# Kernel tuning notes

Hardware: AMD Instinct MI355X
Metric: run time of the kernel (lower is better)

The kernel has to match this reference:

```python
import jax, jax.numpy as jnp
import numpy as np

N, E, C5, C6, H = 50000, 100000, 8000, 12000, 128
RE, R5, R6 = 2 * E, 5 * C5, 6 * C6
BN_EPS = 1e-5


def _bn_relu(x, g, b):
    # BatchNorm1d (training-mode batch stats, biased var) + ReLU
    m = x.mean(0)
    xc = x - m
    v = (xc * xc).mean(0)
    return jax.nn.relu(xc * jax.lax.rsqrt(v + BN_EPS) * g + b)


def _mlp2(x, w1, g1, b1, w2, g2, b2):
    h = _bn_relu(x @ w1, g1, b1)
    return _bn_relu(h @ w2, g2, b2)


def _gather11(x, src_nodes, src_inst, n_inst, tgt_nodes):
    # ptens 1b->1b gather (channel multiplier 2):
    #  part A: identity map on shared atoms, summed over overlapping sources
    #  part B: broadcast of source-instance sum to shared atoms
    pa = jax.ops.segment_sum(x, src_nodes, num_segments=N)[tgt_nodes]
    s = jax.ops.segment_sum(x, src_inst, num_segments=n_inst)
    pb = jax.ops.segment_sum(s[src_inst], src_nodes, num_segments=N)[tgt_nodes]
    return jnp.concatenate([pa, pb], -1)


def _forward(node_rep, edge_rep, cycle_rep, edge_nodes, c5_nodes, c6_nodes, P):
    (nm_w1, nm_g1, nm_b1, nm_w2, nm_g2, nm_b2,
     em_w1, em_g1, em_b1, em_w2, em_g2, em_b2,
     ce_w1, ce_g1, ce_b1, ce_w2, ce_g2, ce_b2,
     cm_w1, cm_g1, cm_b1, cm_w2, cm_g2, cm_b2,
     fm_w, fm_g, fm_b) = P
    edge_inst = jnp.arange(RE, dtype=jnp.int32) // 2
    c5_inst = jnp.arange(R5, dtype=jnp.int32) // 5
    c6_inst = jnp.arange(R6, dtype=jnp.int32) // 6
    cyc_nodes = jnp.concatenate([c5_nodes, c6_nodes])
    cyc_inst = jnp.concatenate([c5_inst, c6_inst + C5])

    # ---- Edge_node ----
    n2e = node_rep[edge_nodes]                                        # 0b->1b(edge), h
    n2e = _gather11(n2e, edge_nodes, edge_inst, E, edge_nodes)        # 2h
    e2e = _gather11(edge_rep, edge_nodes, edge_inst, E, edge_nodes)   # 2h
    e2e = _gather11(e2e, edge_nodes, edge_inst, E, edge_nodes)        # 4h
    e2n = jax.ops.segment_sum(jnp.concatenate([e2e, n2e], -1), edge_nodes, num_segments=N)  # 1b->0b, 6h
    edge_out1 = _mlp2(jnp.concatenate([edge_rep, e2e, n2e], -1),
                      em_w1, em_g1, em_b1, em_w2, em_g2, em_b2)       # [RE, h]
    node_out = _mlp2(jnp.concatenate([node_rep, e2n], -1),
                     nm_w1, nm_g1, nm_b1, nm_w2, nm_g2, nm_b2)        # [N, h]

    # ---- Edge_Cycle ----
    e2c5 = _gather11(edge_rep, edge_nodes, edge_inst, E, c5_nodes)    # 2h
    e2c5 = _gather11(e2c5, c5_nodes, c5_inst, C5, c5_nodes)           # 4h
    e2c6 = _gather11(edge_rep, edge_nodes, edge_inst, E, c6_nodes)    # 2h
    e2c6 = _gather11(e2c6, c6_nodes, c6_inst, C6, c6_nodes)           # 4h
    cycle_in = jnp.concatenate([e2c5, e2c6], 0)                       # row-cat: [R5+R6, 4h]
    cycle_new = jnp.concatenate([cycle_in, cycle_rep], -1)            # 5h
    c2e = _gather11(cycle_new, cyc_nodes, cyc_inst, C5 + C6, edge_nodes)  # 10h
    edge_out2 = _mlp2(jnp.concatenate([edge_rep, c2e], -1),
                      ce_w1, ce_g1, ce_b1, ce_w2, ce_g2, ce_b2)       # [RE, h]
    cycle_out = _mlp2(cycle_new, cm_w1, cm_g1, cm_b1, cm_w2, cm_g2, cm_b2)  # [R5+R6, h]

    edge_out = _bn_relu(jnp.concatenate([edge_out1, edge_out2], -1) @ fm_w, fm_g, fm_b)
    return node_out, edge_out, cycle_out


def setup_inputs() -> dict:
    key = jax.random.key(0)
    ks = jax.random.split(key, 16)
    d = {}
    d["node_rep"] = jax.random.normal(ks[0], (N, H), jnp.float32)
    d["edge_rep"] = jax.random.normal(ks[1], (RE, H), jnp.float32)
    d["cycle_rep"] = jax.random.normal(ks[2], (R5 + R6, H), jnp.float32)
    d["edge_nodes"] = jax.random.randint(ks[3], (RE,), 0, N, jnp.int32)
    d["c5_nodes"] = jax.random.randint(ks[4], (R5,), 0, N, jnp.int32)
    d["c6_nodes"] = jax.random.randint(ks[5], (R6,), 0, N, jnp.int32)
    i = [6]
    def w(shape):
        out = jax.random.normal(ks[i[0]], shape, jnp.float32) / np.float32(np.sqrt(shape[0]))
        i[0] += 1
        return out
    for p, fin in (("nm", 7 * H), ("em", 7 * H), ("ce", 11 * H), ("cm", 5 * H)):
        d[p + "_w1"] = w((fin, 2 * H)); d[p + "_g1"] = jnp.ones((2 * H,), jnp.float32); d[p + "_b1"] = jnp.zeros((2 * H,), jnp.float32)
        d[p + "_w2"] = w((2 * H, H)); d[p + "_g2"] = jnp.ones((H,), jnp.float32); d[p + "_b2"] = jnp.zeros((H,), jnp.float32)
    d["fm_w"] = w((2 * H, H)); d["fm_g"] = jnp.ones((H,), jnp.float32); d["fm_b"] = jnp.zeros((H,), jnp.float32)
    return d


def reference(node_rep, edge_rep, cycle_rep, edge_nodes, c5_nodes, c6_nodes,
              nm_w1, nm_g1, nm_b1, nm_w2, nm_g2, nm_b2,
              em_w1, em_g1, em_b1, em_w2, em_g2, em_b2,
              ce_w1, ce_g1, ce_b1, ce_w2, ce_g2, ce_b2,
              cm_w1, cm_g1, cm_b1, cm_w2, cm_g2, cm_b2,
              fm_w, fm_g, fm_b):
    P = (nm_w1, nm_g1, nm_b1, nm_w2, nm_g2, nm_b2,
         em_w1, em_g1, em_b1, em_w2, em_g2, em_b2,
         ce_w1, ce_g1, ce_b1, ce_w2, ce_g2, ce_b2,
         cm_w1, cm_g1, cm_b1, cm_w2, cm_g2, cm_b2,
         fm_w, fm_g, fm_b)
    return _forward(node_rep, edge_rep, cycle_rep, edge_nodes, c5_nodes, c6_nodes, P)
```

## Files before the change

kernel.cpp:

```cpp
#include <hip/hip_runtime.h>
#include <cstdint>
#include <cstddef>
#include <initializer_list>

typedef short bf16x8 __attribute__((ext_vector_type(8)));
typedef float f32x4 __attribute__((ext_vector_type(4)));

__device__ inline float bf2f(unsigned short h) { return __uint_as_float(((unsigned)h) << 16); }
__device__ inline unsigned short f2bf(float f) {
  unsigned u = __float_as_uint(f);
  u += 0x7fff + ((u >> 16) & 1);
  return (unsigned short)(u >> 16);
}

struct Seg { const void* base; const int* idx; const float* scale; int ld; int wk; int bf16;
             const float* bnsc; const float* bnsh; };
struct GemmArgs { Seg segs[7]; const float* addB; const int* addIdx; float* stats; };

__global__ void k_count(float* dst, const int* __restrict__ idx, int R) {
  int r = blockIdx.x * 256 + threadIdx.x;
  if (r < R) atomicAdd(&dst[idx[r]], 1.0f);
}

__global__ void k_scales(const float* __restrict__ deg, const float* __restrict__ d5,
                         const float* __restrict__ d6, float* deg2, float* dd, int n) {
  int i = blockIdx.x * 256 + threadIdx.x;
  if (i < n) {
    float d = deg[i]; deg2[i] = d * d;
    float a = d5[i], b = d6[i]; dd[i] = a * a + b * b;
  }
}

__global__ void k_wtrans(const float* __restrict__ W, unsigned short* __restrict__ Wt,
                         int K, int CN) {
  int t = blockIdx.x * 256 + threadIdx.x;
  if (t >= K * CN) return;
  int k = t / CN, n = t - k * CN;
  Wt[(size_t)n * K + k] = f2bf(W[t]);
}

__global__ void k_gsum(float* __restrict__ out, int outLd,
                       const float* __restrict__ T, int tLd,
                       const float* __restrict__ scale, const int* __restrict__ idx,
                       int k, int nInst) {
  int t = blockIdx.x * 256 + threadIdx.x;
  int c = t >> 7, ch = t & 127;
  if (c >= nInst) return;
  float acc = 0.f;
  int b0 = c * k;
  for (int j = 0; j < k; ++j) {
    int rid = idx ? idx[b0 + j] : b0 + j;
    float v = T[(size_t)rid * tLd + ch];
    if (scale) v *= scale[rid];
    acc += v;
  }
  out[(size_t)c * outLd + ch] = acc;
}

__global__ void k_scatter(float* __restrict__ dst, const float* __restrict__ src,
                          const int* __restrict__ idx, int R, int C, int div) {
  int r = blockIdx.x;
  if (r >= R) return;
  int n = idx[r];
  const float* s = src + (size_t)(r / div) * C;
  float* d = dst + (size_t)n * C;
  for (int c = threadIdx.x; c < C; c += blockDim.x)
    atomicAdd(&d[c], s[c]);
}

__global__ void k_bnfin(float* __restrict__ coef, const float* __restrict__ stats,
                        const float* __restrict__ g, const float* __restrict__ b,
                        int M, int C) {
  int c = threadIdx.x;
  if (c >= C) return;
  float inv = 1.f / (float)M;
  float m = stats[c] * inv;
  float v = stats[C + c] * inv - m * m;
  float s = g[c] * rsqrtf(v + 1e-5f);
  coef[c] = s;
  coef[C + c] = b[c] - m * s;
}

template <int OUT_BF16>
__launch_bounds__(256)
__global__ void k_gemm(GemmArgs ga, const unsigned short* __restrict__ Wt, int Ktot,
                       int K, int CN, void* __restrict__ Cp, int M) {
  __shared__ char AsB[2 * 128 * 64];
  __shared__ char BsB[2 * 128 * 64];
  int tid = threadIdx.x;
  int row0 = blockIdx.x * 128, col0 = blockIdx.y * 128;
  int l = tid & 63, w = tid >> 6;
  int wm = w >> 1, wn = w & 1;
  int lr = l & 15, g = l >> 4;
  int chunkOff = (g ^ ((lr >> 1) & 3)) << 4;
  int sm = tid >> 2;
  int sc4 = tid & 3;
  f32x4 acc[4][4] = {};

  uint4 pa0[2], pa1[2], pb[2];
  float psc[2];
  float4 c0, c1, c2, c3;

  auto issue = [&](int k0n) {
    Seg sg = ga.segs[k0n >> 7];
    int kin = k0n & 127;
#pragma unroll
    for (int h = 0; h < 2; ++h) {
      int m = sm + 64 * h;
      int grow = row0 + m;
      uint4 z4 = make_uint4(0, 0, 0, 0);
      pa0[h] = z4; pa1[h] = z4; psc[h] = 1.f;
      if (grow < M) {
        int rid = sg.idx ? sg.idx[grow] : grow;
        if (sg.bf16) {
          pa0[h] = *(const uint4*)((const unsigned short*)sg.base + (size_t)rid * sg.ld + kin + sc4 * 8);
        } else {
          const float* fp = (const float*)sg.base + (size_t)rid * sg.ld + kin + sc4 * 8;
          pa0[h] = *(const uint4*)fp;
          pa1[h] = *(const uint4*)(fp + 4);
          if (sg.scale) psc[h] = sg.scale[rid];
        }
      }
      pb[h] = *(const uint4*)(Wt + (size_t)(col0 + m) * Ktot + sg.wk + kin + sc4 * 8);
    }
    if (sg.bnsc) {
      const float* sp = sg.bnsc + kin + sc4 * 8;
      const float* hp = sg.bnsh + kin + sc4 * 8;
      c0 = *(const float4*)sp; c1 = *(const float4*)(sp + 4);
      c2 = *(const float4*)hp; c3 = *(const float4*)(hp + 4);
    }
  };

  issue(0);
  int buf = 0;
  for (int k0 = 0; k0 < K; k0 += 32) {
    {
      Seg sg = ga.segs[k0 >> 7];
      char* sA = AsB + buf * 8192;
      char* sB = BsB + buf * 8192;
#pragma unroll
      for (int h = 0; h < 2; ++h) {
        int m = sm + 64 * h;
        uint4 pk;
        if (sg.bf16) {
          pk = pa0[h];
          if (sg.bnsc) {
            unsigned short* u = (unsigned short*)&pk;
            float cs0[8] = {c0.x, c0.y, c0.z, c0.w, c1.x, c1.y, c1.z, c1.w};
            float sh0[8] = {c2.x, c2.y, c2.z, c2.w, c3.x, c3.y, c3.z, c3.w};
#pragma unroll
            for (int e = 0; e < 8; ++e) {
              float f = fmaxf(0.f, bf2f(u[e]) * cs0[e] + sh0[e]);
              u[e] = f2bf(f);
            }
          }
        } else {
          float4 v0 = *(const float4*)&pa0[h];
          float4 v1 = *(const float4*)&pa1[h];
          float s = psc[h];
          v0.x *= s; v0.y *= s; v0.z *= s; v0.w *= s;
          v1.x *= s; v1.y *= s; v1.z *= s; v1.w *= s;
          if (sg.bnsc) {
            v0.x = fmaxf(0.f, v0.x * c0.x + c2.x);
            v0.y = fmaxf(0.f, v0.y * c0.y + c2.y);
            v0.z = fmaxf(0.f, v0.z * c0.z + c2.z);
            v0.w = fmaxf(0.f, v0.w * c0.w + c2.w);
            v1.x = fmaxf(0.f, v1.x * c1.x + c3.x);
            v1.y = fmaxf(0.f, v1.y * c1.y + c3.y);
            v1.z = fmaxf(0.f, v1.z * c1.z + c3.z);
            v1.w = fmaxf(0.f, v1.w * c1.w + c3.w);
          }
          pk.x = f2bf(v0.x) | ((unsigned)f2bf(v0.y) << 16);
          pk.y = f2bf(v0.z) | ((unsigned)f2bf(v0.w) << 16);
          pk.z = f2bf(v1.x) | ((unsigned)f2bf(v1.y) << 16);
          pk.w = f2bf(v1.z) | ((unsigned)f2bf(v1.w) << 16);
        }
        *(uint4*)(sA + m * 64 + ((sc4 ^ ((m >> 1) & 3)) << 4)) = pk;
        *(uint4*)(sB + m * 64 + ((sc4 ^ ((m >> 1) & 3)) << 4)) = pb[h];
      }
    }
    __syncthreads();
    if (k0 + 32 < K) issue(k0 + 32);
    const char* lA = AsB + buf * 8192;
    const char* lB = BsB + buf * 8192;
    bf16x8 a[4], b4[4];
#pragma unroll
    for (int i = 0; i < 4; ++i) {
      int m = wm * 64 + i * 16 + lr;
      a[i] = *(const bf16x8*)(lA + m * 64 + chunkOff);
    }
#pragma unroll
    for (int j = 0; j < 4; ++j) {
      int n = wn * 64 + j * 16 + lr;
      b4[j] = *(const bf16x8*)(lB + n * 64 + chunkOff);
    }
#pragma unroll
    for (int i = 0; i < 4; ++i)
#pragma unroll
      for (int j = 0; j < 4; ++j)
        acc[i][j] = __builtin_amdgcn_mfma_f32_16x16x32_bf16(a[i], b4[j], acc[i][j], 0, 0, 0);
    buf ^= 1;
  }

  float csum[4] = {0.f, 0.f, 0.f, 0.f}, cqum[4] = {0.f, 0.f, 0.f, 0.f};
#pragma unroll
  for (int i = 0; i < 4; ++i) {
#pragma unroll
    for (int r = 0; r < 4; ++r) {
      int grow = row0 + wm * 64 + i * 16 + g * 4 + r;
      if (grow >= M) continue;
      const float* zr = nullptr;
      if (ga.addB) {
        int rid = ga.addIdx ? ga.addIdx[grow] : grow;
        zr = ga.addB + (size_t)rid * 256;
      }
#pragma unroll
      for (int j = 0; j < 4; ++j) {
        int col = col0 + wn * 64 + j * 16 + lr;
        float o = acc[i][j][r];
        if (zr) o += zr[col];
        csum[j] += o; cqum[j] += o * o;
        if (OUT_BF16) ((unsigned short*)Cp)[(size_t)grow * CN + col] = f2bf(o);
        else          ((float*)Cp)[(size_t)grow * CN + col] = o;
      }
    }
  }
  if (ga.stats) {
#pragma unroll
    for (int j = 0; j < 4; ++j) {
      float s = csum[j], q = cqum[j];
      s += __shfl_xor(s, 16); q += __shfl_xor(q, 16);
      s += __shfl_xor(s, 32); q += __shfl_xor(q, 32);
      if (g == 0) {
        int col = col0 + wn * 64 + j * 16 + lr;
        atomicAdd(&ga.stats[col], s);
        atomicAdd(&ga.stats[CN + col], q);
      }
    }
  }
}

template <int SB, int DB>
__global__ void k_bnapply(void* __restrict__ dst, const void* __restrict__ yv,
                          const float* __restrict__ g, const float* __restrict__ b,
                          const float* __restrict__ stats, int M, int C) {
  int t = blockIdx.x * 256 + threadIdx.x;
  if (t >= M * C) return;
  int c = t & (C - 1);
  float inv = 1.0f / (float)M;
  float m = stats[c] * inv;
  float v = stats[C + c] * inv - m * m;
  float sc = g[c] * rsqrtf(v + 1e-5f);
  float sh = b[c] - m * sc;
  float x = SB ? bf2f(((const unsigned short*)yv)[t]) : ((const float*)yv)[t];
  x = x * sc + sh;
  x = x > 0.f ? x : 0.f;
  if (DB) ((unsigned short*)dst)[t] = f2bf(x);
  else    ((float*)dst)[t] = x;
}

extern "C" void kernel_launch(void* const* d_in, const int* in_sizes, int n_in,
                              void* d_out, int out_size, void* d_ws, size_t ws_size,
                              hipStream_t stream) {
  constexpr int N = 50000, E = 100000, C5 = 8000, C6 = 12000;
  constexpr int RE = 2 * E, R5 = 5 * C5, R6 = 6 * C6, NC = R5 + R6, CC = C5 + C6;

  const float* node_rep  = (const float*)d_in[0];
  const float* edge_rep  = (const float*)d_in[1];
  const float* cycle_rep = (const float*)d_in[2];
  const int* en  = (const int*)d_in[3];
  const int* cn5 = (const int*)d_in[4];
  const int* cn6 = (const int*)d_in[5];
  const float* nm_w1 = (const float*)d_in[6],  *nm_g1 = (const float*)d_in[7],  *nm_b1 = (const float*)d_in[8];
  const float* nm_w2 = (const float*)d_in[9],  *nm_g2 = (const float*)d_in[10], *nm_b2 = (const float*)d_in[11];
  const float* em_w1 = (const float*)d_in[12], *em_g1 = (const float*)d_in[13], *em_b1 = (const float*)d_in[14];
  const float* em_w2 = (const float*)d_in[15], *em_g2 = (const float*)d_in[16], *em_b2 = (const float*)d_in[17];
  const float* ce_w1 = (const float*)d_in[18], *ce_g1 = (const float*)d_in[19], *ce_b1 = (const float*)d_in[20];
  const float* ce_w2 = (const float*)d_in[21], *ce_g2 = (const float*)d_in[22], *ce_b2 = (const float*)d_in[23];
  const float* cm_w1 = (const float*)d_in[24], *cm_g1 = (const float*)d_in[25], *cm_b1 = (const float*)d_in[26];
  const float* cm_w2 = (const float*)d_in[27], *cm_g2 = (const float*)d_in[28], *cm_b2 = (const float*)d_in[29];
  const float* fm_w  = (const float*)d_in[30], *fm_g  = (const float*)d_in[31], *fm_b  = (const float*)d_in[32];
  float* outD = (float*)d_out;
  float* outN = outD;
  float* outE = outD + (size_t)N * 128;
  float* outC = outD + (size_t)(N + RE) * 128;

  char* wsb = (char*)d_ws;
  size_t off = 0;
  auto A = [&](size_t bytes) { void* p = wsb + off; off += (bytes + 255) & ~(size_t)255; return p; };
  float* deg = (float*)A(N * 4);
  float* d5  = (float*)A(N * 4);
  float* d6  = (float*)A(N * 4);
  float* Ae  = (float*)A((size_t)N * 128 * 4);
  float* Be  = (float*)A((size_t)N * 128 * 4);
  float* Bn  = (float*)A((size_t)N * 128 * 4);
  float* pb2 = (float*)A((size_t)N * 256 * 4);
  float* pb5 = (float*)A((size_t)N * 256 * 4);
  float* pb6 = (float*)A((size_t)N * 256 * 4);
  float* Ac  = (float*)A((size_t)N * 128 * 4);
  size_t zeroBytes = off;
  float* deg2 = (float*)A(N * 4);
  float* dd   = (float*)A(N * 4);
  float* Z    = (float*)A((size_t)N * 256 * 4);
  float* stats = (float*)A(512 * 4);
  float* coefCe1 = (float*)A(512 * 4);
  float* coefCe2 = (float*)A(512 * 4);
  float* coefEm1 = (float*)A(512 * 4);
  float* coefEm2 = (float*)A(512 * 4);
  float* coefNm1 = (float*)A(512 * 4);
  float* coefCm1 = (float*)A(512 * 4);
  unsigned short* WtNm1 = (unsigned short*)A((size_t)896 * 256 * 2);
  unsigned short* WtEm1 = (unsigned short*)A((size_t)896 * 256 * 2);
  unsigned short* WtCe1 = (unsigned short*)A((size_t)1408 * 256 * 2);
  unsigned short* WtCm1 = (unsigned short*)A((size_t)640 * 256 * 2);
  unsigned short* WtNm2 = (unsigned short*)A((size_t)256 * 128 * 2);
  unsigned short* WtEm2 = (unsigned short*)A((size_t)256 * 128 * 2);
  unsigned short* WtCe2 = (unsigned short*)A((size_t)256 * 128 * 2);
  unsigned short* WtCm2 = (unsigned short*)A((size_t)256 * 128 * 2);
  unsigned short* WtFm  = (unsigned short*)A((size_t)256 * 128 * 2);
  char*  Yb   = (char*)A((size_t)RE * 256 * 2);
  unsigned short* O2 = (unsigned short*)A((size_t)RE * 128 * 2);
  if (off > ws_size) return;

  float* s2 = (float*)Yb;
  float* sN = s2 + (size_t)E * 128;
  float* s3 = (float*)Yb;
  float* s5 = (float*)Yb;
  float* s6 = s5 + (size_t)C5 * 256;
  float* scb = (float*)Yb;
  float* Ysc = scb + (size_t)CC * 640;

  auto gsum = [&](float* o, int oLd, const float* T, int tLd,
                  const float* scl, const int* idx, int k, int nInst) {
    int tot = nInst * 128;
    k_gsum<<<(tot + 255) / 256, 256, 0, stream>>>(o, oLd, T, tLd, scl, idx, k, nInst);
  };
  auto scat = [&](float* dst, const float* src, const int* idx, int R, int C, int dv) {
    k_scatter<<<R, 128, 0, stream>>>(dst, src, idx, R, C, dv);
  };
  auto wtr = [&](const float* W, unsigned short* Wt, int K, int CN) {
    k_wtrans<<<(K * CN + 255) / 256, 256, 0, stream>>>(W, Wt, K, CN);
  };
  auto gemm = [&](std::initializer_list<Seg> segs, const unsigned short* Wt, int Ktot,
                  int CN, void* Co, int M, bool outBf, const float* addB, const int* addIdx,
                  float* st) {
    GemmArgs ga{}; int i = 0;
    for (const Seg& s : segs) ga.segs[i++] = s;
    ga.addB = addB; ga.addIdx = addIdx; ga.stats = st;
    int K = i * 128;
    dim3 g((M + 127) / 128, CN / 128);
    if (outBf) k_gemm<1><<<g, 256, 0, stream>>>(ga, Wt, Ktot, K, CN, Co, M);
    else       k_gemm<0><<<g, 256, 0, stream>>>(ga, Wt, Ktot, K, CN, Co, M);
  };
  auto zstat = [&](int C) { hipMemsetAsync(stats, 0, 2 * C * sizeof(float), stream); };
  auto fin = [&](float* coef, const float* g, const float* b, int M, int C) {
    k_bnfin<<<1, 256, 0, stream>>>(coef, stats, g, b, M, C);
  };
  auto apply = [&](void* dst, const void* y, const float* g, const float* b,
                   int M, int C, int sb, int db) {
    int tot = M * C, gb = (tot + 255) / 256;
    if (sb && db)       k_bnapply<1, 1><<<gb, 256, 0, stream>>>(dst, y, g, b, stats, M, C);
    else if (sb && !db) k_bnapply<1, 0><<<gb, 256, 0, stream>>>(dst, y, g, b, stats, M, C);
    else if (!sb && db) k_bnapply<0, 1><<<gb, 256, 0, stream>>>(dst, y, g, b, stats, M, C);
    else                k_bnapply<0, 0><<<gb, 256, 0, stream>>>(dst, y, g, b, stats, M, C);
  };

  hipMemsetAsync(d_ws, 0, zeroBytes, stream);
  k_count<<<(RE + 255) / 256, 256, 0, stream>>>(deg, en, RE);
  k_count<<<(R5 + 255) / 256, 256, 0, stream>>>(d5, cn5, R5);
  k_count<<<(R6 + 255) / 256, 256, 0, stream>>>(d6, cn6, R6);
  k_scales<<<(N + 255) / 256, 256, 0, stream>>>(deg, d5, d6, deg2, dd, N);
  wtr(nm_w1, WtNm1, 896, 256);  wtr(em_w1, WtEm1, 896, 256);
  wtr(ce_w1, WtCe1, 1408, 256); wtr(cm_w1, WtCm1, 640, 256);
  wtr(nm_w2, WtNm2, 256, 128);  wtr(em_w2, WtEm2, 256, 128);
  wtr(ce_w2, WtCe2, 256, 128);  wtr(cm_w2, WtCm2, 256, 128);
  wtr(fm_w,  WtFm,  256, 128);

  gsum(s2, 128, edge_rep, 128, nullptr, nullptr, 2, E);
  gsum(sN, 128, node_rep, 128, nullptr, en, 2, E);
  scat(Ae, edge_rep, en, RE, 128, 1);
  scat(Be, s2, en, RE, 128, 2);
  scat(Bn, sN, en, RE, 128, 2);
  gsum(s3, 256, Ae, 128, nullptr, en, 2, E);
  gsum(s3 + 128, 256, Be, 128, nullptr, en, 2, E);
  scat(pb2, s3, en, RE, 256, 2);

  gsum(s5, 256, Ae, 128, nullptr, cn5, 5, C5);
  gsum(s5 + 128, 256, Be, 128, nullptr, cn5, 5, C5);
  gsum(s6, 256, Ae, 128, nullptr, cn6, 6, C6);
  gsum(s6 + 128, 256, Be, 128, nullptr, cn6, 6, C6);
  scat(pb5, s5, cn5, R5, 256, 5);
  scat(pb6, s6, cn6, R6, 256, 6);
  scat(Ac, cycle_rep, cn5, R5, 128, 1);
  scat(Ac, cycle_rep + (size_t)R5 * 128, cn6, R6, 128, 1);

  gsum(scb + 0,   640, Ae, 128, d5, cn5, 5, C5);
  gsum(scb + 128, 640, Be, 128, d5, cn5, 5, C5);
  gsum(scb + 256, 640, pb5, 256, nullptr, cn5, 5, C5);
  gsum(scb + 384, 640, pb5 + 128, 256, nullptr, cn5, 5, C5);
  gsum(scb + 512, 640, cycle_rep, 128, nullptr, nullptr, 5, C5);
  float* sc6 = scb + (size_t)C5 * 640;
  gsum(sc6 + 0,   640, Ae, 128, d6, cn6, 6, C6);
  gsum(sc6 + 128, 640, Be, 128, d6, cn6, 6, C6);
  gsum(sc6 + 256, 640, pb6, 256, nullptr, cn6, 6, C6);
  gsum(sc6 + 384, 640, pb6 + 128, 256, nullptr, cn6, 6, C6);
  gsum(sc6 + 512, 640, cycle_rep + (size_t)R5 * 128, 128, nullptr, nullptr, 6, C6);
  gemm({{scb, nullptr, nullptr, 640, 768, 0}, {scb + 128, nullptr, nullptr, 640, 896, 0},
        {scb + 256, nullptr, nullptr, 640, 1024, 0}, {scb + 384, nullptr, nullptr, 640, 1152, 0},
        {scb + 512, nullptr, nullptr, 640, 1280, 0}},
       WtCe1, 1408, 256, Ysc, CC, false, nullptr, nullptr, nullptr);
  gemm({{Ae, nullptr, dd, 128, 128, 0}, {Be, nullptr, dd, 128, 256, 0},
        {pb5, nullptr, d5, 256, 384, 0}, {pb5 + 128, nullptr, d5, 256, 512, 0},
        {pb6, nullptr, d6, 256, 384, 0}, {pb6 + 128, nullptr, d6, 256, 512, 0},
        {Ac, nullptr, nullptr, 128, 640, 0}},
       WtCe1, 1408, 256, Z, N, false, nullptr, nullptr, nullptr);
  scat(Z, Ysc, cn5, R5, 256, 5);
  scat(Z, Ysc + (size_t)C5 * 256, cn6, R6, 256, 6);
  zstat(256);
  gemm({{edge_rep, nullptr, nullptr, 128, 0, 0}}, WtCe1, 1408, 256, Yb, RE, true, Z, en, stats);
  fin(coefCe1, ce_g1, ce_b1, RE, 256);
  zstat(128);
  gemm({{Yb, nullptr, nullptr, 256, 0, 1, coefCe1, coefCe1 + 256},
        {Yb + 256, nullptr, nullptr, 256, 128, 1, coefCe1 + 128, coefCe1 + 384}},
       WtCe2, 256, 128, O2, RE, true, nullptr, nullptr, stats);
  fin(coefCe2, ce_g2, ce_b2, RE, 128);

  gemm({{Ae, nullptr, deg, 128, 128, 0}, {Be, nullptr, deg, 128, 256, 0},
        {pb2, nullptr, nullptr, 256, 384, 0}, {pb2 + 128, nullptr, nullptr, 256, 512, 0},
        {node_rep, nullptr, deg, 128, 640, 0}, {Bn, nullptr, nullptr, 128, 768, 0}},
       WtEm1, 896, 256, Z, N, false, nullptr, nullptr, nullptr);
  zstat(256);
  gemm({{edge_rep, nullptr, nullptr, 128, 0, 0}}, WtEm1, 896, 256, Yb, RE, true, Z, en, stats);
  fin(coefEm1, em_g1, em_b1, RE, 256);
  zstat(128);
  gemm({{Yb, nullptr, nullptr, 256, 0, 1, coefEm1, coefEm1 + 256},
        {Yb + 256, nullptr, nullptr, 256, 128, 1, coefEm1 + 128, coefEm1 + 384}},
       WtEm2, 256, 128, outE, RE, false, nullptr, nullptr, stats);
  fin(coefEm2, em_g2, em_b2, RE, 128);

  zstat(256);
  gemm({{node_rep, nullptr, nullptr, 128, 0, 0}, {Ae, nullptr, deg2, 128, 128, 0},
        {Be, nullptr, deg2, 128, 256, 0}, {pb2, nullptr, deg, 256, 384, 0},
        {pb2 + 128, nullptr, deg, 256, 512, 0}, {node_rep, nullptr, deg2, 128, 640, 0},
        {Bn, nullptr, deg, 128, 768, 0}},
       WtNm1, 896, 256, Yb, N, true, nullptr, nullptr, stats);
  fin(coefNm1, nm_g1, nm_b1, N, 256);
  zstat(128);
  gemm({{Yb, nullptr, nullptr, 256, 0, 1, coefNm1, coefNm1 + 256},
        {Yb + 256, nullptr, nullptr, 256, 128, 1, coefNm1 + 128, coefNm1 + 384}},
       WtNm2, 256, 128, outN, N, false, nullptr, nullptr, stats);
  apply(outN, outN, nm_g2, nm_b2, N, 128, 0, 0);

  gemm({{Ae, nullptr, d5, 128, 0, 0}, {Be, nullptr, d5, 128, 128, 0},
        {pb5, nullptr, nullptr, 256, 256, 0}, {pb5 + 128, nullptr, nullptr, 256, 384, 0}},
       WtCm1, 640, 256, Z, N, false, nullptr, nullptr, nullptr);
  zstat(256);
  gemm({{cycle_rep, nullptr, nullptr, 128, 512, 0}}, WtCm1, 640, 256, Yb, R5, true, Z, cn5, stats);
  gemm({{Ae, nullptr, d6, 128, 0, 0}, {Be, nullptr, d6, 128, 128, 0},
        {pb6, nullptr, nullptr, 256, 256, 0}, {pb6 + 128, nullptr, nullptr, 256, 384, 0}},
       WtCm1, 640, 256, Z, N, false, nullptr, nullptr, nullptr);
  gemm({{cycle_rep + (size_t)R5 * 128, nullptr, nullptr, 128, 512, 0}}, WtCm1, 640, 256,
       Yb + (size_t)R5 * 256 * 2, R6, true, Z, cn6, stats);
  fin(coefCm1, cm_g1, cm_b1, NC, 256);
  zstat(128);
  gemm({{Yb, nullptr, nullptr, 256, 0, 1, coefCm1, coefCm1 + 256},
        {Yb + 256, nullptr, nullptr, 256, 128, 1, coefCm1 + 128, coefCm1 + 384}},
       WtCm2, 256, 128, outC, NC, false, nullptr, nullptr, stats);
  apply(outC, outC, cm_g2, cm_b2, NC, 128, 0, 0);

  zstat(128);
  gemm({{outE, nullptr, nullptr, 128, 0, 0, coefEm2, coefEm2 + 128},
        {O2, nullptr, nullptr, 128, 128, 1, coefCe2, coefCe2 + 128}},
       WtFm, 256, 128, Yb, RE, true, nullptr, nullptr, stats);
  apply(outE, Yb, fm_g, fm_b, RE, 128, 1, 0);
}
```

Measured before the change: 3.385 ms.

## Shard BN stat atomics, store gather tables in bf16, fuse gather-sum-scatter kernels

```diff
diff --git a/kernel.cpp b/kernel.cpp
--- a/kernel.cpp
+++ b/kernel.cpp
@@ -15,7 +15,7 @@
 
 struct Seg { const void* base; const int* idx; const float* scale; int ld; int wk; int bf16;
              const float* bnsc; const float* bnsh; };
-struct GemmArgs { Seg segs[7]; const float* addB; const int* addIdx; float* stats; };
+struct GemmArgs { Seg segs[7]; const float* addB; const int* addIdx; float* stats; int addBf16; };
 
 __global__ void k_count(float* dst, const int* __restrict__ idx, int R) {
   int r = blockIdx.x * 256 + threadIdx.x;
@@ -37,6 +37,17 @@
   if (t >= K * CN) return;
   int k = t / CN, n = t - k * CN;
   Wt[(size_t)n * K + k] = f2bf(W[t]);
+}
+
+__global__ void k_cvt(unsigned short* __restrict__ dst, const float* __restrict__ src, int n8) {
+  int i = blockIdx.x * 256 + threadIdx.x;
+  if (i >= n8) return;
+  const float4* s = (const float4*)(src + (size_t)i * 8);
+  float4 a = s[0], b = s[1];
+  union { unsigned short u[8]; uint4 v; } o;
+  o.u[0] = f2bf(a.x); o.u[1] = f2bf(a.y); o.u[2] = f2bf(a.z); o.u[3] = f2bf(a.w);
+  o.u[4] = f2bf(b.x); o.u[5] = f2bf(b.y); o.u[6] = f2bf(b.z); o.u[7] = f2bf(b.w);
+  *(uint4*)(dst + (size_t)i * 8) = o.v;
 }
 
 __global__ void k_gsum(float* __restrict__ out, int outLd,
@@ -57,6 +68,26 @@
   out[(size_t)c * outLd + ch] = acc;
 }
 
+__global__ void k_gsc(float* __restrict__ dst, const float* __restrict__ T1,
+                      const float* __restrict__ T2, const int* __restrict__ gidx,
+                      const int* __restrict__ sidx, int k, int nInst, int cshift) {
+  int t = blockIdx.x * 256 + threadIdx.x;
+  int c = t >> cshift;
+  int C = 1 << cshift;
+  int ch = t & (C - 1);
+  if (c >= nInst) return;
+  const float* T = (ch < 128) ? T1 : T2;
+  int ch7 = ch & 127;
+  float acc = 0.f;
+  int b0 = c * k;
+  for (int j = 0; j < k; ++j) {
+    int rid = gidx ? gidx[b0 + j] : b0 + j;
+    acc += T[(size_t)rid * 128 + ch7];
+  }
+  for (int j = 0; j < k; ++j)
+    atomicAdd(&dst[(size_t)sidx[b0 + j] * C + ch], acc);
+}
+
 __global__ void k_scatter(float* __restrict__ dst, const float* __restrict__ src,
                           const int* __restrict__ idx, int R, int C, int div) {
   int r = blockIdx.x;
@@ -73,12 +104,14 @@
                         int M, int C) {
   int c = threadIdx.x;
   if (c >= C) return;
+  float s = 0.f, q = 0.f;
+  for (int sh = 0; sh < 16; ++sh) { s += stats[sh * 512 + c]; q += stats[sh * 512 + 256 + c]; }
   float inv = 1.f / (float)M;
-  float m = stats[c] * inv;
-  float v = stats[C + c] * inv - m * m;
-  float s = g[c] * rsqrtf(v + 1e-5f);
-  coef[c] = s;
-  coef[C + c] = b[c] - m * s;
+  float m = s * inv;
+  float v = q * inv - m * m;
+  float sc = g[c] * rsqrtf(v + 1e-5f);
+  coef[c] = sc;
+  coef[C + c] = b[c] - m * sc;
 }
 
 template <int OUT_BF16>
@@ -209,16 +242,19 @@
     for (int r = 0; r < 4; ++r) {
       int grow = row0 + wm * 64 + i * 16 + g * 4 + r;
       if (grow >= M) continue;
-      const float* zr = nullptr;
+      const float* zrF = nullptr;
+      const unsigned short* zrH = nullptr;
       if (ga.addB) {
         int rid = ga.addIdx ? ga.addIdx[grow] : grow;
-        zr = ga.addB + (size_t)rid * 256;
+        if (ga.addBf16) zrH = (const unsigned short*)ga.addB + (size_t)rid * 256;
+        else            zrF = ga.addB + (size_t)rid * 256;
       }
 #pragma unroll
       for (int j = 0; j < 4; ++j) {
         int col = col0 + wn * 64 + j * 16 + lr;
         float o = acc[i][j][r];
-        if (zr) o += zr[col];
+        if (zrF) o += zrF[col];
+        if (zrH) o += bf2f(zrH[col]);
         csum[j] += o; cqum[j] += o * o;
         if (OUT_BF16) ((unsigned short*)Cp)[(size_t)grow * CN + col] = f2bf(o);
         else          ((float*)Cp)[(size_t)grow * CN + col] = o;
@@ -226,6 +262,7 @@
     }
   }
   if (ga.stats) {
+    int shard = (blockIdx.x & 15) * 512;
 #pragma unroll
     for (int j = 0; j < 4; ++j) {
       float s = csum[j], q = cqum[j];
@@ -233,8 +270,8 @@
       s += __shfl_xor(s, 32); q += __shfl_xor(q, 32);
       if (g == 0) {
         int col = col0 + wn * 64 + j * 16 + lr;
-        atomicAdd(&ga.stats[col], s);
-        atomicAdd(&ga.stats[CN + col], q);
+        atomicAdd(&ga.stats[shard + col], s);
+        atomicAdd(&ga.stats[shard + 256 + col], q);
       }
     }
   }
@@ -242,18 +279,12 @@
 
 template <int SB, int DB>
 __global__ void k_bnapply(void* __restrict__ dst, const void* __restrict__ yv,
-                          const float* __restrict__ g, const float* __restrict__ b,
-                          const float* __restrict__ stats, int M, int C) {
+                          const float* __restrict__ coef, int M, int C) {
   int t = blockIdx.x * 256 + threadIdx.x;
   if (t >= M * C) return;
   int c = t & (C - 1);
-  float inv = 1.0f / (float)M;
-  float m = stats[c] * inv;
-  float v = stats[C + c] * inv - m * m;
-  float sc = g[c] * rsqrtf(v + 1e-5f);
-  float sh = b[c] - m * sc;
   float x = SB ? bf2f(((const unsigned short*)yv)[t]) : ((const float*)yv)[t];
-  x = x * sc + sh;
+  x = x * coef[c] + coef[C + c];
   x = x > 0.f ? x : 0.f;
   if (DB) ((unsigned short*)dst)[t] = f2bf(x);
   else    ((float*)dst)[t] = x;
@@ -302,13 +333,16 @@
   float* deg2 = (float*)A(N * 4);
   float* dd   = (float*)A(N * 4);
   float* Z    = (float*)A((size_t)N * 256 * 4);
-  float* stats = (float*)A(512 * 4);
+  float* stats = (float*)A(16 * 512 * 4);
   float* coefCe1 = (float*)A(512 * 4);
   float* coefCe2 = (float*)A(512 * 4);
   float* coefEm1 = (float*)A(512 * 4);
   float* coefEm2 = (float*)A(512 * 4);
   float* coefNm1 = (float*)A(512 * 4);
+  float* coefNm2 = (float*)A(512 * 4);
   float* coefCm1 = (float*)A(512 * 4);
+  float* coefCm2 = (float*)A(512 * 4);
+  float* coefFm  = (float*)A(512 * 4);
   unsigned short* WtNm1 = (unsigned short*)A((size_t)896 * 256 * 2);
   unsigned short* WtEm1 = (unsigned short*)A((size_t)896 * 256 * 2);
   unsigned short* WtCe1 = (unsigned short*)A((size_t)1408 * 256 * 2);
@@ -322,11 +356,8 @@
   unsigned short* O2 = (unsigned short*)A((size_t)RE * 128 * 2);
   if (off > ws_size) return;
 
-  float* s2 = (float*)Yb;
-  float* sN = s2 + (size_t)E * 128;
-  float* s3 = (float*)Yb;
-  float* s5 = (float*)Yb;
-  float* s6 = s5 + (size_t)C5 * 256;
+  unsigned short* Zb = (unsigned short*)Ac;
+
   float* scb = (float*)Yb;
   float* Ysc = scb + (size_t)CC * 640;
 
@@ -335,6 +366,12 @@
     int tot = nInst * 128;
     k_gsum<<<(tot + 255) / 256, 256, 0, stream>>>(o, oLd, T, tLd, scl, idx, k, nInst);
   };
+  auto gsc = [&](float* dst, const float* T1, const float* T2, const int* gidx,
+                 const int* sidx, int k, int nInst) {
+    int cshift = T2 ? 8 : 7;
+    int tot = nInst << cshift;
+    k_gsc<<<(tot + 255) / 256, 256, 0, stream>>>(dst, T1, T2, gidx, sidx, k, nInst, cshift);
+  };
   auto scat = [&](float* dst, const float* src, const int* idx, int R, int C, int dv) {
     k_scatter<<<R, 128, 0, stream>>>(dst, src, idx, R, C, dv);
   };
@@ -343,26 +380,25 @@
   };
   auto gemm = [&](std::initializer_list<Seg> segs, const unsigned short* Wt, int Ktot,
                   int CN, void* Co, int M, bool outBf, const float* addB, const int* addIdx,
-                  float* st) {
+                  int addBf, float* st) {
     GemmArgs ga{}; int i = 0;
     for (const Seg& s : segs) ga.segs[i++] = s;
-    ga.addB = addB; ga.addIdx = addIdx; ga.stats = st;
+    ga.addB = addB; ga.addIdx = addIdx; ga.stats = st; ga.addBf16 = addBf;
     int K = i * 128;
     dim3 g((M + 127) / 128, CN / 128);
     if (outBf) k_gemm<1><<<g, 256, 0, stream>>>(ga, Wt, Ktot, K, CN, Co, M);
     else       k_gemm<0><<<g, 256, 0, stream>>>(ga, Wt, Ktot, K, CN, Co, M);
   };
-  auto zstat = [&](int C) { hipMemsetAsync(stats, 0, 2 * C * sizeof(float), stream); };
+  auto zstat = [&]() { hipMemsetAsync(stats, 0, 16 * 512 * sizeof(float), stream); };
   auto fin = [&](float* coef, const float* g, const float* b, int M, int C) {
     k_bnfin<<<1, 256, 0, stream>>>(coef, stats, g, b, M, C);
   };
-  auto apply = [&](void* dst, const void* y, const float* g, const float* b,
-                   int M, int C, int sb, int db) {
+  auto apply = [&](void* dst, const void* y, const float* coef, int M, int C, int sb, int db) {
     int tot = M * C, gb = (tot + 255) / 256;
-    if (sb && db)       k_bnapply<1, 1><<<gb, 256, 0, stream>>>(dst, y, g, b, stats, M, C);
-    else if (sb && !db) k_bnapply<1, 0><<<gb, 256, 0, stream>>>(dst, y, g, b, stats, M, C);
-    else if (!sb && db) k_bnapply<0, 1><<<gb, 256, 0, stream>>>(dst, y, g, b, stats, M, C);
-    else                k_bnapply<0, 0><<<gb, 256, 0, stream>>>(dst, y, g, b, stats, M, C);
+    if (sb && db)       k_bnapply<1, 1><<<gb, 256, 0, stream>>>(dst, y, coef, M, C);
+    else if (sb && !db) k_bnapply<1, 0><<<gb, 256, 0, stream>>>(dst, y, coef, M, C);
+    else if (!sb && db) k_bnapply<0, 1><<<gb, 256, 0, stream>>>(dst, y, coef, M, C);
+    else                k_bnapply<0, 0><<<gb, 256, 0, stream>>>(dst, y, coef, M, C);
   };
 
   hipMemsetAsync(d_ws, 0, zeroBytes, stream);
@@ -376,21 +412,13 @@
   wtr(ce_w2, WtCe2, 256, 128);  wtr(cm_w2, WtCm2, 256, 128);
   wtr(fm_w,  WtFm,  256, 128);
 
-  gsum(s2, 128, edge_rep, 128, nullptr, nullptr, 2, E);
-  gsum(sN, 128, node_rep, 128, nullptr, en, 2, E);
   scat(Ae, edge_rep, en, RE, 128, 1);
-  scat(Be, s2, en, RE, 128, 2);
-  scat(Bn, sN, en, RE, 128, 2);
-  gsum(s3, 256, Ae, 128, nullptr, en, 2, E);
-  gsum(s3 + 128, 256, Be, 128, nullptr, en, 2, E);
-  scat(pb2, s3, en, RE, 256, 2);
-
-  gsum(s5, 256, Ae, 128, nullptr, cn5, 5, C5);
-  gsum(s5 + 128, 256, Be, 128, nullptr, cn5, 5, C5);
-  gsum(s6, 256, Ae, 128, nullptr, cn6, 6, C6);
-  gsum(s6 + 128, 256, Be, 128, nullptr, cn6, 6, C6);
-  scat(pb5, s5, cn5, R5, 256, 5);
-  scat(pb6, s6, cn6, R6, 256, 6);
+  gsc(Be, edge_rep, nullptr, nullptr, en, 2, E);
+  gsc(Bn, node_rep, nullptr, en, en, 2, E);
+  gsc(pb2, Ae, Be, en, en, 2, E);
+
+  gsc(pb5, Ae, Be, cn5, cn5, 5, C5);
+  gsc(pb6, Ae, Be, cn6, cn6, 6, C6);
   scat(Ac, cycle_rep, cn5, R5, 128, 1);
   scat(Ac, cycle_rep + (size_t)R5 * 128, cn6, R6, 128, 1);
 
@@ -408,69 +436,76 @@
   gemm({{scb, nullptr, nullptr, 640, 768, 0}, {scb + 128, nullptr, nullptr, 640, 896, 0},
         {scb + 256, nullptr, nullptr, 640, 1024, 0}, {scb + 384, nullptr, nullptr, 640, 1152, 0},
         {scb + 512, nullptr, nullptr, 640, 1280, 0}},
-       WtCe1, 1408, 256, Ysc, CC, false, nullptr, nullptr, nullptr);
+       WtCe1, 1408, 256, Ysc, CC, false, nullptr, nullptr, 0, nullptr);
   gemm({{Ae, nullptr, dd, 128, 128, 0}, {Be, nullptr, dd, 128, 256, 0},
         {pb5, nullptr, d5, 256, 384, 0}, {pb5 + 128, nullptr, d5, 256, 512, 0},
         {pb6, nullptr, d6, 256, 384, 0}, {pb6 + 128, nullptr, d6, 256, 512, 0},
         {Ac, nullptr, nullptr, 128, 640, 0}},
-       WtCe1, 1408, 256, Z, N, false, nullptr, nullptr, nullptr);
+       WtCe1, 1408, 256, Z, N, false, nullptr, nullptr, 0, nullptr);
   scat(Z, Ysc, cn5, R5, 256, 5);
   scat(Z, Ysc + (size_t)C5 * 256, cn6, R6, 256, 6);
-  zstat(256);
-  gemm({{edge_rep, nullptr, nullptr, 128, 0, 0}}, WtCe1, 1408, 256, Yb, RE, true, Z, en, stats);
+  k_cvt<<<(N * 256 / 8 + 255) / 256, 256, 0, stream>>>(Zb, Z, N * 256 / 8);
+  zstat();
+  gemm({{edge_rep, nullptr, nullptr, 128, 0, 0}}, WtCe1, 1408, 256, Yb, RE, true,
+       (const float*)Zb, en, 1, stats);
   fin(coefCe1, ce_g1, ce_b1, RE, 256);
-  zstat(128);
+  zstat();
   gemm({{Yb, nullptr, nullptr, 256, 0, 1, coefCe1, coefCe1 + 256},
         {Yb + 256, nullptr, nullptr, 256, 128, 1, coefCe1 + 128, coefCe1 + 384}},
-       WtCe2, 256, 128, O2, RE, true, nullptr, nullptr, stats);
+       WtCe2, 256, 128, O2, RE, true, nullptr, nullptr, 0, stats);
   fin(coefCe2, ce_g2, ce_b2, RE, 128);
 
   gemm({{Ae, nullptr, deg, 128, 128, 0}, {Be, nullptr, deg, 128, 256, 0},
         {pb2, nullptr, nullptr, 256, 384, 0}, {pb2 + 128, nullptr, nullptr, 256, 512, 0},
         {node_rep, nullptr, deg, 128, 640, 0}, {Bn, nullptr, nullptr, 128, 768, 0}},
-       WtEm1, 896, 256, Z, N, false, nullptr, nullptr, nullptr);
-  zstat(256);
-  gemm({{edge_rep, nullptr, nullptr, 128, 0, 0}}, WtEm1, 896, 256, Yb, RE, true, Z, en, stats);
+       WtEm1, 896, 256, Zb, N, true, nullptr, nullptr, 0, nullptr);
+  zstat();
+  gemm({{edge_rep, nullptr, nullptr, 128, 0, 0}}, WtEm1, 896, 256, Yb, RE, true,
+       (const float*)Zb, en, 1, stats);
   fin(coefEm1, em_g1, em_b1, RE, 256);
-  zstat(128);
+  zstat();
   gemm({{Yb, nullptr, nullptr, 256, 0, 1, coefEm1, coefEm1 + 256},
         {Yb + 256, nullptr, nullptr, 256, 128, 1, coefEm1 + 128, coefEm1 + 384}},
-       WtEm2, 256, 128, outE, RE, false, nullptr, nullptr, stats);
+       WtEm2, 256, 128, outE, RE, false, nullptr, nullptr, 0, stats);
   fin(coefEm2, em_g2, em_b2, RE, 128);
 
-  zstat(256);
+  zstat();
   gemm({{node_rep, nullptr, nullptr, 128, 0, 0}, {Ae, nullptr, deg2, 128, 128, 0},
         {Be, nullptr, deg2, 128, 256, 0}, {pb2, nullptr, deg, 256, 384, 0},
         {pb2 + 128, nullptr, deg, 256, 512, 0}, {node_rep, nullptr, deg2, 128, 640, 0},
         {Bn, nullptr, deg, 128, 768, 0}},
-       WtNm1, 896, 256, Yb, N, true, nullptr, nullptr, stats);
+       WtNm1, 896, 256, Yb, N, true, nullptr, nullptr, 0, stats);
   fin(coefNm1, nm_g1, nm_b1, N, 256);
-  zstat(128);
+  zstat();
   gemm({{Yb, nullptr, nullptr, 256, 0, 1, coefNm1, coefNm1 + 256},
         {Yb + 256, nullptr, nullptr, 256, 128, 1, coefNm1 + 128, coefNm1 + 384}},
-       WtNm2, 256, 128, outN, N, false, nullptr, nullptr, stats);
-  apply(outN, outN, nm_g2, nm_b2, N, 128, 0, 0);
+       WtNm2, 256, 128, outN, N, false, nullptr, nullptr, 0, stats);
+  fin(coefNm2, nm_g2, nm_b2, N, 128);
+  apply(outN, outN, coefNm2, N, 128, 0, 0);
 
   gemm({{Ae, nullptr, d5, 128, 0, 0}, {Be, nullptr, d5, 128, 128, 0},
         {pb5, nullptr, nullptr, 256, 256, 0}, {pb5 + 128, nullptr, nullptr, 256, 384, 0}},
-       WtCm1, 640, 256, Z, N, false, nullptr, nullptr, nullptr);
-  zstat(256);
-  gemm({{cycle_rep, nullptr, nullptr, 128, 512, 0}}, WtCm1, 640, 256, Yb, R5, true, Z, cn5, stats);
+       WtCm1, 640, 256, Zb, N, true, nullptr, nullptr, 0, nullptr);
+  zstat();
+  gemm({{cycle_rep, nullptr, nullptr, 128, 512, 0}}, WtCm1, 640, 256, Yb, R5, true,
+       (const float*)Zb, cn5, 1, stats);
   gemm({{Ae, nullptr, d6, 128, 0, 0}, {Be, nullptr, d6, 128, 128, 0},
         {pb6, nullptr, nullptr, 256, 256, 0}, {pb6 + 128, nullptr, nullptr, 256, 384, 0}},
-       WtCm1, 640, 256, Z, N, false, nullptr, nullptr, nullptr);
+       WtCm1, 640, 256, Zb, N, true, nullptr, nullptr, 0, nullptr);
   gemm({{cycle_rep + (size_t)R5 * 128, nullptr, nullptr, 128, 512, 0}}, WtCm1, 640, 256,
-       Yb + (size_t)R5 * 256 * 2, R6, true, Z, cn6, stats);
+       Yb + (size_t)R5 * 256 * 2, R6, true, (const float*)Zb, cn6, 1, stats);
   fin(coefCm1, cm_g1, cm_b1, NC, 256);
-  zstat(128);
+  zstat();
   gemm({{Yb, nullptr, nullptr, 256, 0, 1, coefCm1, coefCm1 + 256},
         {Yb + 256, nullptr, nullptr, 256, 128, 1, coefCm1 + 128, coefCm1 + 384}},
-       WtCm2, 256, 128, outC, NC, false, nullptr, nullptr, stats);
-  apply(outC, outC, cm_g2, cm_b2, NC, 128, 0, 0);
-
-  zstat(128);
+       WtCm2, 256, 128, outC, NC, false, nullptr, nullptr, 0, stats);
+  fin(coefCm2, cm_g2, cm_b2, NC, 128);
+  apply(outC, outC, coefCm2, NC, 128, 0, 0);
+
+  zstat();
   gemm({{outE, nullptr, nullptr, 128, 0, 0, coefEm2, coefEm2 + 128},
         {O2, nullptr, nullptr, 128, 128, 1, coefCe2, coefCe2 + 128}},
-       WtFm, 256, 128, Yb, RE, true, nullptr, nullptr, stats);
-  apply(outE, Yb, fm_g, fm_b, RE, 128, 1, 0);
-}
+       WtFm, 256, 128, Yb, RE, true, nullptr, nullptr, 0, stats);
+  fin(coefFm, fm_g, fm_b, RE, 128);
+  apply(outE, Yb, coefFm, RE, 128, 1, 0);
+}
```

Result: faster. 2.871 ms (-15.2%).
